# Kernel tuning notes

Measured on AMD Instinct MI355X. Metric: run time of the kernel, lower is better.

Reference implementation:

```python
import math
import jax, jax.numpy as jnp
import numpy as np

B, S, D, H, L, V = 2, 1024, 1024, 16, 6, 256
HD = D // H  # 64
PAD = 0


def setup_inputs() -> dict:
    key = jax.random.key(0)
    ks = jax.random.split(key, 22)
    s = 0.02
    f32 = jnp.float32
    inp = {
        "x": jax.random.randint(ks[0], (B, S), 0, V, dtype=jnp.int32),
        "emb": (jax.random.normal(ks[1], (V, D)) * s).astype(f32),
        "Wq": (jax.random.normal(ks[2], (L, D, D)) * s).astype(f32),
        "bq": jnp.zeros((L, D), f32),
        "Wk": (jax.random.normal(ks[3], (L, D, D)) * s).astype(f32),
        "bk": jnp.zeros((L, D), f32),
        "Wv": (jax.random.normal(ks[4], (L, D, D)) * s).astype(f32),
        "bv": jnp.zeros((L, D), f32),
        "Wo": (jax.random.normal(ks[5], (L, D, D)) * s).astype(f32),
        "bo": jnp.zeros((L, D), f32),
        "W1": (jax.random.normal(ks[6], (L, D, D // 2)) * s).astype(f32),
        "b1": jnp.zeros((L, D // 2), f32),
        "W2": (jax.random.normal(ks[7], (L, D // 2, D)) * s).astype(f32),
        "b2": jnp.zeros((L, D), f32),
        "g1": jnp.ones((L, D), f32),
        "be1": jnp.zeros((L, D), f32),
        "g2": jnp.ones((L, D), f32),
        "be2": jnp.zeros((L, D), f32),
        "E": jax.random.normal(ks[8], (L, S, HD)).astype(f32),  # relative pos embeddings, non-trainable
        "Wf": (jax.random.normal(ks[9], (D, V)) * s).astype(f32),
        "bf": jnp.zeros((V,), f32),
    }
    return inp


def _layernorm(x, g, b, eps=1e-6):
    mu = jnp.mean(x, axis=-1, keepdims=True)
    var = jnp.mean((x - mu) ** 2, axis=-1, keepdims=True)
    return (x - mu) * jax.lax.rsqrt(var + eps) * g + b


def _pos_encoding():
    # embed[p, i] = sin(p * exp(-ln(1e4)*i/D) * exp(ln(1e4)*(i%2)/D) + 0.5*pi*(i%2))
    i = jnp.arange(D, dtype=jnp.float32)
    par = jnp.mod(i, 2.0)
    rate = jnp.exp(-math.log(10000.0) * i / D) * jnp.exp(math.log(10000.0) * par / D)
    pos = jnp.arange(S, dtype=jnp.float32)
    return jnp.sin(pos[:, None] * rate[None, :] + 0.5 * math.pi * par[None, :])  # [S, D]


def _skew(QE):
    # Music Transformer skewing: pad one col on the left, reshape, drop first row.
    padded = jnp.pad(QE, ((0, 0), (0, 0), (0, 0), (1, 0)))  # [B,H,S,S+1]
    reshaped = padded.reshape(B, H, S + 1, S)
    return reshaped[:, :, 1:, :]  # [B,H,S,S]


def reference(x, emb, Wq, bq, Wk, bk, Wv, bv, Wo, bo, W1, b1, W2, b2,
              g1, be1, g2, be2, E, Wf, bf):
    pe = _pos_encoding()
    # look-ahead mask: pad positions OR strictly-future positions
    pad_mask = (x == PAD)[:, None, None, :]                      # [B,1,1,S]
    causal = jnp.triu(jnp.ones((S, S), bool), k=1)[None, None]   # [1,1,S,S]
    neg = (pad_mask | causal).astype(jnp.float32) * -1e9         # [B,1,S,S]
    # QE mask: keep qe[i, j] only where j >= S-1-i (upper-right triangle)
    idx = jnp.arange(S)
    qe_mask = (idx[None, :] >= (S - 1 - idx)[:, None]).astype(jnp.float32)

    h = emb[x] * math.sqrt(D) + pe[None]  # [B,S,D]
    scale = 1.0 / math.sqrt(HD)
    for l in range(L):
        q = (h @ Wq[l] + bq[l]).reshape(B, S, H, HD).transpose(0, 2, 1, 3)
        k = (h @ Wk[l] + bk[l]).reshape(B, S, H, HD).transpose(0, 2, 1, 3)
        v = (h @ Wv[l] + bv[l]).reshape(B, S, H, HD).transpose(0, 2, 1, 3)
        QE = jnp.einsum('bhld,md->bhlm', q, E[l]) * qe_mask
        Srel = _skew(QE)
        logits = (jnp.einsum('bhld,bhmd->bhlm', q, k) + Srel) * scale + neg
        aw = jax.nn.softmax(logits, axis=-1)
        attn = jnp.einsum('bhlm,bhmd->bhld', aw, v)
        attn = attn.transpose(0, 2, 1, 3).reshape(B, S, D)
        ao = attn @ Wo[l] + bo[l]
        o1 = _layernorm(ao, g1[l], be1[l])          # NOTE: no residual, as in source
        f = jax.nn.relu(o1 @ W1[l] + b1[l]) @ W2[l] + b2[l]
        h = _layernorm(f, g2[l], be2[l])
    return h @ Wf + bf  # [B,S,V]
```

## Files before the change

kernel.cpp:

```cpp
#include <hip/hip_runtime.h>
#include <hip/hip_bf16.h>


typedef __attribute__((ext_vector_type(8))) short  s8_t;
typedef __attribute__((ext_vector_type(4))) short  s4_t;
typedef __attribute__((ext_vector_type(8))) __bf16 bf8_t;
typedef __attribute__((ext_vector_type(4))) float  f4v;

static __device__ __forceinline__ short f2bf(float f) {
  union { float f; unsigned u; } a; a.f = f;
  unsigned u = a.u;
  u += 0x7fffu + ((u >> 16) & 1u);
  return (short)(u >> 16);
}
static __device__ __forceinline__ float bf2f(short s) {
  union { float f; unsigned u; } a;
  a.u = ((unsigned)(unsigned short)s) << 16;
  return a.f;
}
static __device__ __forceinline__ f4v mfma16(s8_t a, s8_t b, f4v c) {
  return __builtin_amdgcn_mfma_f32_16x16x32_bf16(
      __builtin_bit_cast(bf8_t, a), __builtin_bit_cast(bf8_t, b), c, 0, 0, 0);
}
static __device__ __forceinline__ void gld16(const short* g, short* l) {
  __builtin_amdgcn_global_load_lds(
      (const __attribute__((address_space(1))) void*)g,
      (__attribute__((address_space(3))) void*)l, 16, 0, 0);
}

static __device__ const int IT_TAB[40] = {
  15,15,15,15, 14,14,14,14, 13,13,13,13, 12,12,12,12,
  11,11,11, 10,10,10, 9,9,9, 8,8,8,
  7,7, 6,6, 5,5, 4,4, 3, 2, 1, 0};
static __device__ const int CW_TAB[40] = {
  0,1,2,3, 0,1,2,3, 0,1,2,3, 0,1,2,3,
  0,1,2, 0,1,2, 0,1,2, 0,1,2,
  0,1, 0,1, 0,1, 0,1, 0, 0, 0, 0};

__global__ void prep_weights(
    const float* __restrict__ Wq, const float* __restrict__ Wk,
    const float* __restrict__ Wv, const float* __restrict__ Wo,
    const float* __restrict__ W1, const float* __restrict__ W2,
    const float* __restrict__ Wf,
    short* __restrict__ qkvT, short* __restrict__ WoT, short* __restrict__ W1T,
    short* __restrict__ W2T, short* __restrict__ WfT) {
  __shared__ float tile[32][33];
  int z = blockIdx.x;
  const float* in; short* out; int R, C; long outBS; int rowOff = 0;
  if (z < 18432) {
    R = 1024; C = 1024; outBS = (long)3072 * 1024; out = qkvT;
    if (z < 6144)       { in = Wq; }
    else if (z < 12288) { in = Wk; rowOff = 1024; z -= 6144; }
    else                { in = Wv; rowOff = 2048; z -= 12288; }
  } else if (z < 24576) { in = Wo; out = WoT; R = 1024; C = 1024; outBS = (long)1024 * 1024; z -= 18432; }
  else if (z < 27648)   { in = W1; out = W1T; R = 1024; C = 512;  outBS = (long)512 * 1024;  z -= 24576; }
  else if (z < 30720)   { in = W2; out = W2T; R = 512;  C = 1024; outBS = (long)1024 * 512;  z -= 27648; }
  else                  { in = Wf; out = WfT; R = 1024; C = 256;  outBS = 0;                 z -= 30720; }
  const int nx = C >> 5, ny = R >> 5;
  const int per = nx * ny;
  const int l = z / per, rem = z % per;
  const int cx = rem % nx, cy = rem / nx;
  in += (long)l * R * C;
  out += (long)l * outBS + (long)rowOff * R;
  const int c0 = cx * 32, r0 = cy * 32;
  const int tx = threadIdx.x, ty = threadIdx.y;
#pragma unroll
  for (int i = 0; i < 4; i++)
    tile[ty + i * 8][tx] = in[(long)(r0 + ty + i * 8) * C + c0 + tx];
  __syncthreads();
#pragma unroll
  for (int i = 0; i < 4; i++)
    out[(long)(c0 + ty + i * 8) * R + r0 + tx] = f2bf(tile[tx][ty + i * 8]);
}

__global__ __launch_bounds__(256) void prep_misc(
    const int* __restrict__ x, const float* __restrict__ emb,
    const float* __restrict__ E,
    const float* __restrict__ bq, const float* __restrict__ bk,
    const float* __restrict__ bv,
    short* __restrict__ h, short* __restrict__ Ebf,
    float* __restrict__ qkvB, int* __restrict__ fnp) {
  const int z = blockIdx.x;
  const int tid = threadIdx.x;
  if (z < 2048) {
    const int s = z & 1023;
    const int xv = x[z];
    const int c = tid << 2;
    const float4 e = *(const float4*)(emb + (long)xv * 1024 + c);
    const float ev[4] = {e.x, e.y, e.z, e.w};
    s4_t o;
#pragma unroll
    for (int i = 0; i < 4; i++) {
      const int d = c + i;
      const float par = (float)(d & 1);
      const float rate = expf(-9.210340371976184f * (float)d / 1024.0f) *
                         expf(9.210340371976184f * par / 1024.0f);
      const float pe = sinf((float)s * rate + 1.5707963267948966f * par);
      o[i] = f2bf(ev[i] * 32.0f + pe);
    }
    *(s4_t*)(h + (long)z * 1024 + c) = o;
  } else if (z < 2432) {
    const long i = ((long)(z - 2048) * 256 + tid) * 4;
    const float4 t = *(const float4*)(E + i);
    s4_t o = {f2bf(t.x), f2bf(t.y), f2bf(t.z), f2bf(t.w)};
    *(s4_t*)(Ebf + i) = o;
  } else if (z < 2504) {
    const int idx = (z - 2432) * 256 + tid;
    const int l = idx / 3072, n = idx % 3072;
    float v = (n < 1024) ? bq[l * 1024 + n]
            : (n < 2048) ? bk[l * 1024 + n - 1024]
                         : bv[l * 1024 + n - 2048];
    qkvB[idx] = v;
  } else {
    if (tid < 64) {
      const int b = z - 2504;
      int first = 1024;
      for (int j0 = 0; j0 < 1024; j0 += 64) {
        unsigned long long m = __ballot(x[b * 1024 + j0 + tid] != 0);
        if (m) { first = j0 + __ffsll(m) - 1; break; }
      }
      if (tid == 0) fnp[b] = first;
    }
  }
}

__global__ __launch_bounds__(256) void ln_kernel(const short* __restrict__ in,
                                                 short* __restrict__ out,
                                                 const float* __restrict__ g,
                                                 const float* __restrict__ be) {
  __shared__ float red[4];
  __shared__ float red2[4];
  const int row = blockIdx.x;
  const int tid = threadIdx.x;
  const int c = tid << 2;
  const s4_t xv = *(const s4_t*)(in + (long)row * 1024 + c);
  const float x0 = bf2f(xv[0]), x1 = bf2f(xv[1]), x2 = bf2f(xv[2]), x3 = bf2f(xv[3]);
  float s = x0 + x1 + x2 + x3;
#pragma unroll
  for (int off = 1; off < 64; off <<= 1) s += __shfl_xor(s, off);
  const int wave = tid >> 6, lane = tid & 63;
  if (lane == 0) red[wave] = s;
  __syncthreads();
  const float mu = (red[0] + red[1] + red[2] + red[3]) * (1.0f / 1024.0f);
  const float d0 = x0 - mu, d1 = x1 - mu, d2 = x2 - mu, d3 = x3 - mu;
  float q = d0 * d0 + d1 * d1 + d2 * d2 + d3 * d3;
#pragma unroll
  for (int off = 1; off < 64; off <<= 1) q += __shfl_xor(q, off);
  if (lane == 0) red2[wave] = q;
  __syncthreads();
  const float var = (red2[0] + red2[1] + red2[2] + red2[3]) * (1.0f / 1024.0f);
  const float rs = rsqrtf(var + 1e-6f);
  const float4 gv = *(const float4*)(g + c);
  const float4 bv = *(const float4*)(be + c);
  s4_t o = {f2bf(d0 * rs * gv.x + bv.x), f2bf(d1 * rs * gv.y + bv.y),
            f2bf(d2 * rs * gv.z + bv.z), f2bf(d3 * rs * gv.w + bv.w)};
  *(s4_t*)(out + (long)row * 1024 + c) = o;
}

template <int BM, int BN, int WR, int WC, int OUT_BF16, int RELU>
__global__ __launch_bounds__(256) void gemm_lds(
    const short* __restrict__ A, const short* __restrict__ BT,
    void* __restrict__ Cv, const float* __restrict__ biasp,
    int K, int lda, int ldb, int ldc) {
  constexpr int AR = BM / 64, BR = BN / 64;
  constexpr int FI = BM / WR / 16, FJ = BN / WC / 16;
  __shared__ short As[BM * 32];
  __shared__ short Bs[BN * 32];
  const int bm = blockIdx.y * BM, bn = blockIdx.x * BN;
  const int tid = threadIdx.x;
  const int wave = tid >> 6, lane = tid & 63;
  const int quad = lane >> 4, l16 = lane & 15;
  const int wr = wave / WC, wc = wave % WC;
  const int wm = wr * (BM / WR), wn = wc * (BN / WC);

  const short* Ag = A + (long)(bm + wave * 16 + (lane >> 2)) * lda + ((lane & 3) << 3);
  const short* Bg = BT + (long)(bn + wave * 16 + (lane >> 2)) * ldb + ((lane & 3) << 3);

  f4v acc[FI][FJ];
#pragma unroll
  for (int i = 0; i < FI; i++)
#pragma unroll
    for (int j = 0; j < FJ; j++) {
      f4v zz = {0.f, 0.f, 0.f, 0.f};
      acc[i][j] = zz;
    }

  for (int k0 = 0; k0 < K; k0 += 32) {
#pragma unroll
    for (int r = 0; r < AR; r++)
      gld16(Ag + (long)r * 64 * lda + k0, As + r * 2048 + wave * 512);
#pragma unroll
    for (int r = 0; r < BR; r++)
      gld16(Bg + (long)r * 64 * ldb + k0, Bs + r * 2048 + wave * 512);
    __syncthreads();
    s8_t af[FI], bfr[FJ];
#pragma unroll
    for (int t = 0; t < FI; t++)
      af[t] = *(const s8_t*)&As[(wm + t * 16 + l16) * 32 + quad * 8];
#pragma unroll
    for (int t = 0; t < FJ; t++)
      bfr[t] = *(const s8_t*)&Bs[(wn + t * 16 + l16) * 32 + quad * 8];
#pragma unroll
    for (int ti = 0; ti < FI; ti++)
#pragma unroll
      for (int tj = 0; tj < FJ; tj++)
        acc[ti][tj] = mfma16(af[ti], bfr[tj], acc[ti][tj]);
    __syncthreads();
  }

#pragma unroll
  for (int ti = 0; ti < FI; ti++) {
#pragma unroll
    for (int tj = 0; tj < FJ; tj++) {
      const int n = bn + wn + tj * 16 + l16;
      const float bval = biasp ? biasp[n] : 0.f;
#pragma unroll
      for (int r = 0; r < 4; r++) {
        const int m = bm + wm + ti * 16 + quad * 4 + r;
        float vv = acc[ti][tj][r] + bval;
        if (RELU) vv = fmaxf(vv, 0.f);
        if (OUT_BF16) ((short*)Cv)[(long)m * ldc + n] = f2bf(vv);
        else          ((float*)Cv)[(long)m * ldc + n] = vv;
      }
    }
  }
}

__global__ __launch_bounds__(256) void attn_main(
    const short* __restrict__ qkv, const short* __restrict__ Eb,
    const int* __restrict__ xids, const int* __restrict__ fnp,
    float* __restrict__ PO, float* __restrict__ PM, float* __restrict__ PL,
    short* __restrict__ outb) {
  __shared__ short Ks2[8][64][8];
  __shared__ short Vt[64][72];
  __shared__ short Gs[4][16][88];
  __shared__ float kneg[64];

  const int bh = blockIdx.x, b = bh >> 4, hh = bh & 15;
  const int yy = blockIdx.y;
  const bool fbp = (yy >= 40);
  const int itile = fbp ? (yy - 40) : IT_TAB[yy];
  const int cw = fbp ? 0 : CW_TAB[yy];
  const int fb = fnp[b];
  const int i0g = itile * 64;
  if (fbp && fb <= i0g) return;

  const int tid = threadIdx.x;
  const int wave = tid >> 6, lane = tid & 63, quad = lane >> 4, l16 = lane & 15;
  const int i0 = i0g + wave * 16;

  s8_t aq[2];
  {
    const short* qp = qkv + ((long)(b * 1024 + i0 + l16)) * 3072 + hh * 64 + quad * 8;
    aq[0] = *(const s8_t*)qp;
    aq[1] = *(const s8_t*)(qp + 32);
  }

  f4v o[4];
#pragma unroll
  for (int nt = 0; nt < 4; nt++) { f4v zz = {0.f, 0.f, 0.f, 0.f}; o[nt] = zz; }
  float m_run[4] = {-INFINITY, -INFINITY, -INFINITY, -INFINITY};
  float l_run[4] = {0.f, 0.f, 0.f, 0.f};

  const short* kbase = qkv + (long)b * 1024 * 3072 + 1024 + hh * 64 + wave * 8;
  const short* vbase = qkv + (long)b * 1024 * 3072 + 2048 + hh * 64 + wave * 16;
  short* gs = &Gs[wave][0][0];

  const int jBeg = fbp ? 0 : cw * 256;
  const int jEnd = fbp ? 1024 : min(cw * 256 + 256, i0g + 64);

  for (int j0 = jBeg; j0 < jEnd; j0 += 64) {
    {
      const long k1 = min(j0 + lane, 1023);
      gld16(kbase + k1 * 3072, &Ks2[wave][0][0]);
      gld16(kbase + k1 * 3072 + 32, &Ks2[wave + 4][0][0]);
      const short* vrow = vbase + k1 * 3072;
      const s8_t v0 = *(const s8_t*)(vrow);
      const s8_t v1 = *(const s8_t*)(vrow + 8);
#pragma unroll
      for (int t = 0; t < 8; t++) {
        Vt[wave * 16 + t][lane] = v0[t];
        Vt[wave * 16 + 8 + t][lane] = v1[t];
      }
    }
    if (tid < 64) kneg[tid] = (xids[b * 1024 + min(j0 + tid, 1023)] == 0) ? -1e9f : 0.0f;

    {
      const int mW = 1008 - i0g - wave * 16 + j0;
#pragma unroll
      for (int t = 0; t < 5; t++) {
        const int m = min(mW + t * 16 + l16, 1023);
        const short* ep = Eb + m * 64 + quad * 8;
        const s8_t eb0 = *(const s8_t*)ep;
        const s8_t eb1 = *(const s8_t*)(ep + 32);
        f4v g = {0.f, 0.f, 0.f, 0.f};
        g = mfma16(aq[0], eb0, g);
        g = mfma16(aq[1], eb1, g);
#pragma unroll
        for (int r = 0; r < 4; r++)
          gs[(quad * 4 + r) * 88 + t * 16 + l16] = f2bf(g[r]);
      }
    }
    __syncthreads();

    float p[4][4];
    const int irow = i0 + quad * 4;
#pragma unroll
    for (int jt = 0; jt < 4; jt++) {
      const s8_t k0f = *(const s8_t*)&Ks2[quad][jt * 16 + l16][0];
      const s8_t k1f = *(const s8_t*)&Ks2[4 + quad][jt * 16 + l16][0];
      f4v zz = {0.f, 0.f, 0.f, 0.f};
      zz = mfma16(aq[0], k0f, zz);
      zz = mfma16(aq[1], k1f, zz);
      const int j = j0 + jt * 16 + l16;
      const float kn = kneg[jt * 16 + l16];
#pragma unroll
      for (int r = 0; r < 4; r++) {
        const int rr = quad * 4 + r;
        const float smv = bf2f(gs[rr * 87 + 15 + jt * 16 + l16]);
        const bool causal = (j <= irow + r);
        const float srel = causal ? smv : 0.f;
        const float kk = fbp ? 0.f : (causal ? kn : -1e9f);
        p[jt][r] = (zz[r] + srel) * 0.125f + kk;
      }
    }

    float alpha[4];
#pragma unroll
    for (int r = 0; r < 4; r++) {
      float mx = p[0][r];
#pragma unroll
      for (int jt = 1; jt < 4; jt++) mx = fmaxf(mx, p[jt][r]);
      mx = fmaxf(mx, __shfl_xor(mx, 1));
      mx = fmaxf(mx, __shfl_xor(mx, 2));
      mx = fmaxf(mx, __shfl_xor(mx, 4));
      mx = fmaxf(mx, __shfl_xor(mx, 8));
      const float mnew = fmaxf(m_run[r], mx);
      alpha[r] = __expf(m_run[r] - mnew);
      float ps = 0.f;
#pragma unroll
      for (int jt = 0; jt < 4; jt++) {
        p[jt][r] = __expf(p[jt][r] - mnew);
        ps += p[jt][r];
      }
      ps += __shfl_xor(ps, 1);
      ps += __shfl_xor(ps, 2);
      ps += __shfl_xor(ps, 4);
      ps += __shfl_xor(ps, 8);
      l_run[r] = l_run[r] * alpha[r] + ps;
      m_run[r] = mnew;
    }

#pragma unroll
    for (int jt = 0; jt < 4; jt++)
#pragma unroll
      for (int r = 0; r < 4; r++)
        gs[(quad * 4 + r) * 88 + jt * 16 + l16] = f2bf(p[jt][r]);
#pragma unroll
    for (int nt = 0; nt < 4; nt++)
#pragma unroll
      for (int r = 0; r < 4; r++)
        o[nt][r] *= alpha[r];

#pragma unroll
    for (int ks4 = 0; ks4 < 2; ks4++) {
      const s8_t ap = *(const s8_t*)&gs[l16 * 88 + ks4 * 32 + quad * 8];
#pragma unroll
      for (int nt = 0; nt < 4; nt++) {
        const s8_t vf = *(const s8_t*)&Vt[nt * 16 + l16][ks4 * 32 + quad * 8];
        o[nt] = mfma16(ap, vf, o[nt]);
      }
    }
    __syncthreads();
  }

  if (fbp) {
#pragma unroll
    for (int nt = 0; nt < 4; nt++)
#pragma unroll
      for (int r = 0; r < 4; r++) {
        const int i = i0 + quad * 4 + r;
        if (i < fb)
          outb[((long)(b * 1024 + i)) * 1024 + hh * 64 + nt * 16 + l16] =
              f2bf(o[nt][r] / l_run[r]);
      }
  } else if (yy >= 36) {
#pragma unroll
    for (int nt = 0; nt < 4; nt++)
#pragma unroll
      for (int r = 0; r < 4; r++) {
        const int i = i0 + quad * 4 + r;
        if (i >= fb)
          outb[((long)(b * 1024 + i)) * 1024 + hh * 64 + nt * 16 + l16] =
              f2bf(o[nt][r] / l_run[r]);
      }
  } else {
    const long part = (long)(bh * 16 + itile) * 4 + cw;
    float* po = PO + part * 4096;
#pragma unroll
    for (int nt = 0; nt < 4; nt++)
#pragma unroll
      for (int r = 0; r < 4; r++) {
        const int row = wave * 16 + quad * 4 + r;
        po[row * 64 + nt * 16 + l16] = o[nt][r];
      }
    if (l16 == 0) {
#pragma unroll
      for (int r = 0; r < 4; r++) {
        const int row = wave * 16 + quad * 4 + r;
        PM[part * 64 + row] = m_run[r];
        PL[part * 64 + row] = l_run[r];
      }
    }
  }
}

__global__ __launch_bounds__(256) void attn_combine(
    const float* __restrict__ PO, const float* __restrict__ PM,
    const float* __restrict__ PL, const int* __restrict__ fnp,
    short* __restrict__ outb) {
  const int id = blockIdx.x;
  const int bh = id / 12, itile = 4 + id % 12;
  const int b = bh >> 4, hh = bh & 15;
  const int nc = (itile >> 2) + 1;
  const int row = threadIdx.x >> 2, seg = (threadIdx.x & 3) << 4;
  const long base = (long)(bh * 16 + itile) * 4;
  const int i = itile * 64 + row;
  if (i < fnp[b]) return;

  float mv[4];
  float M = -INFINITY;
  for (int c = 0; c < nc; c++) {
    mv[c] = PM[(base + c) * 64 + row];
    M = fmaxf(M, mv[c]);
  }
  f4v acc[4];
#pragma unroll
  for (int t = 0; t < 4; t++) { f4v zz = {0.f, 0.f, 0.f, 0.f}; acc[t] = zz; }
  float l = 0.f;
  for (int c = 0; c < nc; c++) {
    const float w = __expf(mv[c] - M);
    l += w * PL[(base + c) * 64 + row];
    const float* po = PO + (base + c) * 4096 + row * 64 + seg;
#pragma unroll
    for (int t = 0; t < 4; t++) {
      const f4v v = *(const f4v*)(po + t * 4);
      acc[t] += w * v;
    }
  }
  const float inv = 1.0f / l;
  short* op = outb + ((long)(b * 1024 + i)) * 1024 + hh * 64 + seg;
#pragma unroll
  for (int t = 0; t < 4; t++) {
    s4_t o = {f2bf(acc[t][0] * inv), f2bf(acc[t][1] * inv),
              f2bf(acc[t][2] * inv), f2bf(acc[t][3] * inv)};
    *(s4_t*)(op + t * 4) = o;
  }
}

extern "C" void kernel_launch(void* const* d_in, const int* in_sizes, int n_in,
                              void* d_out, int out_size, void* d_ws, size_t ws_size,
                              hipStream_t stream) {
  const int*   x   = (const int*)d_in[0];
  const float* emb = (const float*)d_in[1];
  const float* Wq  = (const float*)d_in[2];
  const float* bq  = (const float*)d_in[3];
  const float* Wk  = (const float*)d_in[4];
  const float* bk  = (const float*)d_in[5];
  const float* Wv  = (const float*)d_in[6];
  const float* bv  = (const float*)d_in[7];
  const float* Wo  = (const float*)d_in[8];
  const float* bo  = (const float*)d_in[9];
  const float* W1  = (const float*)d_in[10];
  const float* b1  = (const float*)d_in[11];
  const float* W2  = (const float*)d_in[12];
  const float* b2  = (const float*)d_in[13];
  const float* g1  = (const float*)d_in[14];
  const float* be1 = (const float*)d_in[15];
  const float* g2  = (const float*)d_in[16];
  const float* be2 = (const float*)d_in[17];
  const float* E   = (const float*)d_in[18];
  const float* Wf  = (const float*)d_in[19];
  const float* bfv = (const float*)d_in[20];

  char* p = (char*)d_ws;
  auto alloc = [&](size_t bytes) {
    char* r = p;
    p += (bytes + 255) & ~(size_t)255;
    return r;
  };
  short* h    = (short*)alloc(2048ull * 1024 * 2);
  short* qkv  = (short*)alloc(2048ull * 3072 * 2);
  short* attn = (short*)alloc(2048ull * 1024 * 2);
  short* tmp  = (short*)alloc(2048ull * 1024 * 2);
  short* mid  = (short*)alloc(2048ull * 512 * 2);
  short* qkvT = (short*)alloc(6ull * 3072 * 1024 * 2);
  short* WoT  = (short*)alloc(6ull * 1024 * 1024 * 2);
  short* W1T  = (short*)alloc(6ull * 512 * 1024 * 2);
  short* W2T  = (short*)alloc(6ull * 1024 * 512 * 2);
  short* WfT  = (short*)alloc(256ull * 1024 * 2);
  short* Ebf  = (short*)alloc(6ull * 1024 * 64 * 2);
  float* qkvB = (float*)alloc(6ull * 3072 * 4);
  int*   fnp  = (int*)alloc(256);
  float* PO   = (float*)alloc(2048ull * 4096 * 4);
  float* PM   = (float*)alloc(2048ull * 64 * 4);
  float* PL   = (float*)alloc(2048ull * 64 * 4);

  prep_weights<<<30976, dim3(32, 8), 0, stream>>>(
      Wq, Wk, Wv, Wo, W1, W2, Wf, qkvT, WoT, W1T, W2T, WfT);
  prep_misc<<<2506, 256, 0, stream>>>(x, emb, E, bq, bk, bv, h, Ebf, qkvB, fnp);

  for (int l = 0; l < 6; l++) {
    const long wOff = (long)l * 1024 * 1024;
    const long w12Off = (long)l * 512 * 1024;
    gemm_lds<128, 128, 2, 2, 1, 0><<<dim3(24, 16), 256, 0, stream>>>(
        h, qkvT + (long)l * 3072 * 1024, qkv, qkvB + l * 3072, 1024, 1024, 1024, 3072);
    attn_main<<<dim3(32, 56), 256, 0, stream>>>(
        qkv, Ebf + (long)l * 1024 * 64, x, fnp, PO, PM, PL, attn);
    attn_combine<<<384, 256, 0, stream>>>(PO, PM, PL, fnp, attn);
    gemm_lds<64, 64, 2, 2, 1, 0><<<dim3(16, 32), 256, 0, stream>>>(
        attn, WoT + wOff, tmp, bo + l * 1024, 1024, 1024, 1024, 1024);
    ln_kernel<<<2048, 256, 0, stream>>>(tmp, tmp, g1 + l * 1024, be1 + l * 1024);
    gemm_lds<64, 64, 2, 2, 1, 1><<<dim3(8, 32), 256, 0, stream>>>(
        tmp, W1T + w12Off, mid, b1 + l * 512, 1024, 1024, 1024, 512);
    gemm_lds<64, 64, 2, 2, 1, 0><<<dim3(16, 32), 256, 0, stream>>>(
        mid, W2T + w12Off, h, b2 + l * 1024, 512, 512, 512, 1024);
    ln_kernel<<<2048, 256, 0, stream>>>(h, h, g2 + l * 1024, be2 + l * 1024);
  }
  gemm_lds<64, 64, 2, 2, 0, 0><<<dim3(4, 32), 256, 0, stream>>>(
      h, WfT, (float*)d_out, bfv, 1024, 1024, 1024, 256);
}
```

Baseline: 968.4 us.

## Double-buffer K/V tiles in attention and widen weight-transpose tiles

The attention kernel now double-buffers the K tile in shared memory and prefetches the next V rows into registers while the current tile is computed, so global loads overlap with MFMA work. The key-padding mask is precomputed once per block as a bf16 array covering the whole sequence instead of being reloaded every iteration. The weight-prep transpose moves to 64x64 tiles with float4 loads and 16-byte bf16 stores, cutting the block count. This costs more LDS and registers per block, which could lower occupancy, and the bf16 mask value of -1e9 is no longer exact.

```diff
diff --git a/kernel.cpp b/kernel.cpp
--- a/kernel.cpp
+++ b/kernel.cpp
@@ -37,40 +37,54 @@
   0,1,2, 0,1,2, 0,1,2, 0,1,2,
   0,1, 0,1, 0,1, 0,1, 0, 0, 0, 0};
 
-__global__ void prep_weights(
+__global__ __launch_bounds__(256) void prep_weights(
     const float* __restrict__ Wq, const float* __restrict__ Wk,
     const float* __restrict__ Wv, const float* __restrict__ Wo,
     const float* __restrict__ W1, const float* __restrict__ W2,
     const float* __restrict__ Wf,
     short* __restrict__ qkvT, short* __restrict__ WoT, short* __restrict__ W1T,
     short* __restrict__ W2T, short* __restrict__ WfT) {
-  __shared__ float tile[32][33];
+  __shared__ float tile[64][69];
   int z = blockIdx.x;
   const float* in; short* out; int R, C; long outBS; int rowOff = 0;
-  if (z < 18432) {
+  if (z < 4608) {
     R = 1024; C = 1024; outBS = (long)3072 * 1024; out = qkvT;
-    if (z < 6144)       { in = Wq; }
-    else if (z < 12288) { in = Wk; rowOff = 1024; z -= 6144; }
-    else                { in = Wv; rowOff = 2048; z -= 12288; }
-  } else if (z < 24576) { in = Wo; out = WoT; R = 1024; C = 1024; outBS = (long)1024 * 1024; z -= 18432; }
-  else if (z < 27648)   { in = W1; out = W1T; R = 1024; C = 512;  outBS = (long)512 * 1024;  z -= 24576; }
-  else if (z < 30720)   { in = W2; out = W2T; R = 512;  C = 1024; outBS = (long)1024 * 512;  z -= 27648; }
-  else                  { in = Wf; out = WfT; R = 1024; C = 256;  outBS = 0;                 z -= 30720; }
-  const int nx = C >> 5, ny = R >> 5;
+    if (z < 1536)      { in = Wq; }
+    else if (z < 3072) { in = Wk; rowOff = 1024; z -= 1536; }
+    else               { in = Wv; rowOff = 2048; z -= 3072; }
+  } else if (z < 6144) { in = Wo; out = WoT; R = 1024; C = 1024; outBS = (long)1024 * 1024; z -= 4608; }
+  else if (z < 6912)   { in = W1; out = W1T; R = 1024; C = 512;  outBS = (long)512 * 1024;  z -= 6144; }
+  else if (z < 7680)   { in = W2; out = W2T; R = 512;  C = 1024; outBS = (long)1024 * 512;  z -= 6912; }
+  else                 { in = Wf; out = WfT; R = 1024; C = 256;  outBS = 0;                 z -= 7680; }
+  const int nx = C >> 6, ny = R >> 6;
   const int per = nx * ny;
   const int l = z / per, rem = z % per;
   const int cx = rem % nx, cy = rem / nx;
   in += (long)l * R * C;
   out += (long)l * outBS + (long)rowOff * R;
-  const int c0 = cx * 32, r0 = cy * 32;
-  const int tx = threadIdx.x, ty = threadIdx.y;
-#pragma unroll
-  for (int i = 0; i < 4; i++)
-    tile[ty + i * 8][tx] = in[(long)(r0 + ty + i * 8) * C + c0 + tx];
+  const int c0 = cx * 64, r0 = cy * 64;
+  const int tid = threadIdx.x;
+
+  const int lr = tid >> 4, lc4 = tid & 15;
+#pragma unroll
+  for (int p = 0; p < 4; p++) {
+    const int row = p * 16 + lr;
+    const float4 v = *(const float4*)(in + (long)(r0 + row) * C + c0 + lc4 * 4);
+    tile[row][lc4 * 4 + 0] = v.x;
+    tile[row][lc4 * 4 + 1] = v.y;
+    tile[row][lc4 * 4 + 2] = v.z;
+    tile[row][lc4 * 4 + 3] = v.w;
+  }
   __syncthreads();
-#pragma unroll
-  for (int i = 0; i < 4; i++)
-    out[(long)(c0 + ty + i * 8) * R + r0 + tx] = f2bf(tile[tx][ty + i * 8]);
+  const int seg = tid & 7;
+#pragma unroll
+  for (int q = 0; q < 2; q++) {
+    const int oc = q * 32 + (tid >> 3);
+    s8_t o;
+#pragma unroll
+    for (int j = 0; j < 8; j++) o[j] = f2bf(tile[seg * 8 + j][oc]);
+    *(s8_t*)(out + (long)(c0 + oc) * R + r0 + seg * 8) = o;
+  }
 }
 
 __global__ __launch_bounds__(256) void prep_misc(
@@ -231,10 +245,10 @@
     const int* __restrict__ xids, const int* __restrict__ fnp,
     float* __restrict__ PO, float* __restrict__ PM, float* __restrict__ PL,
     short* __restrict__ outb) {
-  __shared__ short Ks2[8][64][8];
+  __shared__ short Ks2[2][8][64][8];
   __shared__ short Vt[64][72];
   __shared__ short Gs[4][16][88];
-  __shared__ float kneg[64];
+  __shared__ short knegs[1024];
 
   const int bh = blockIdx.x, b = bh >> 4, hh = bh & 15;
   const int yy = blockIdx.y;
@@ -249,6 +263,15 @@
   const int wave = tid >> 6, lane = tid & 63, quad = lane >> 4, l16 = lane & 15;
   const int i0 = i0g + wave * 16;
 
+  {
+    const short neg = f2bf(-1e9f);
+#pragma unroll
+    for (int t = 0; t < 4; t++) {
+      const int idx = t * 256 + tid;
+      knegs[idx] = (xids[b * 1024 + idx] == 0) ? neg : (short)0;
+    }
+  }
+
   s8_t aq[2];
   {
     const short* qp = qkv + ((long)(b * 1024 + i0 + l16)) * 3072 + hh * 64 + quad * 8;
@@ -269,21 +292,25 @@
   const int jBeg = fbp ? 0 : cw * 256;
   const int jEnd = fbp ? 1024 : min(cw * 256 + 256, i0g + 64);
 
+  s8_t vr0, vr1;
+  {
+    const long k1 = min(jBeg + lane, 1023);
+    gld16(kbase + k1 * 3072, &Ks2[0][wave][0][0]);
+    gld16(kbase + k1 * 3072 + 32, &Ks2[0][wave + 4][0][0]);
+    const short* vrow = vbase + k1 * 3072;
+    vr0 = *(const s8_t*)(vrow);
+    vr1 = *(const s8_t*)(vrow + 8);
+#pragma unroll
+    for (int t = 0; t < 8; t++) {
+      Vt[wave * 16 + t][lane] = vr0[t];
+      Vt[wave * 16 + 8 + t][lane] = vr1[t];
+    }
+  }
+
+  int pb = 0;
   for (int j0 = jBeg; j0 < jEnd; j0 += 64) {
-    {
-      const long k1 = min(j0 + lane, 1023);
-      gld16(kbase + k1 * 3072, &Ks2[wave][0][0]);
-      gld16(kbase + k1 * 3072 + 32, &Ks2[wave + 4][0][0]);
-      const short* vrow = vbase + k1 * 3072;
-      const s8_t v0 = *(const s8_t*)(vrow);
-      const s8_t v1 = *(const s8_t*)(vrow + 8);
-#pragma unroll
-      for (int t = 0; t < 8; t++) {
-        Vt[wave * 16 + t][lane] = v0[t];
-        Vt[wave * 16 + 8 + t][lane] = v1[t];
-      }
-    }
-    if (tid < 64) kneg[tid] = (xids[b * 1024 + min(j0 + tid, 1023)] == 0) ? -1e9f : 0.0f;
+    const bool hasNext = (j0 + 64 < jEnd);
+    __syncthreads();
 
     {
       const int mW = 1008 - i0g - wave * 16 + j0;
@@ -301,19 +328,27 @@
           gs[(quad * 4 + r) * 88 + t * 16 + l16] = f2bf(g[r]);
       }
     }
-    __syncthreads();
+
+    if (hasNext) {
+      const long k1 = min(j0 + 64 + lane, 1023);
+      gld16(kbase + k1 * 3072, &Ks2[pb ^ 1][wave][0][0]);
+      gld16(kbase + k1 * 3072 + 32, &Ks2[pb ^ 1][wave + 4][0][0]);
+      const short* vrow = vbase + k1 * 3072;
+      vr0 = *(const s8_t*)(vrow);
+      vr1 = *(const s8_t*)(vrow + 8);
+    }
 
     float p[4][4];
     const int irow = i0 + quad * 4;
 #pragma unroll
     for (int jt = 0; jt < 4; jt++) {
-      const s8_t k0f = *(const s8_t*)&Ks2[quad][jt * 16 + l16][0];
-      const s8_t k1f = *(const s8_t*)&Ks2[4 + quad][jt * 16 + l16][0];
+      const s8_t k0f = *(const s8_t*)&Ks2[pb][quad][jt * 16 + l16][0];
+      const s8_t k1f = *(const s8_t*)&Ks2[pb][4 + quad][jt * 16 + l16][0];
       f4v zz = {0.f, 0.f, 0.f, 0.f};
       zz = mfma16(aq[0], k0f, zz);
       zz = mfma16(aq[1], k1f, zz);
       const int j = j0 + jt * 16 + l16;
-      const float kn = kneg[jt * 16 + l16];
+      const float kn = bf2f(knegs[j]);
 #pragma unroll
       for (int r = 0; r < 4; r++) {
         const int rr = quad * 4 + r;
@@ -371,7 +406,16 @@
         o[nt] = mfma16(ap, vf, o[nt]);
       }
     }
+
     __syncthreads();
+    if (hasNext) {
+#pragma unroll
+      for (int t = 0; t < 8; t++) {
+        Vt[wave * 16 + t][lane] = vr0[t];
+        Vt[wave * 16 + 8 + t][lane] = vr1[t];
+      }
+    }
+    pb ^= 1;
   }
 
   if (fbp) {
@@ -506,7 +550,7 @@
   float* PM   = (float*)alloc(2048ull * 64 * 4);
   float* PL   = (float*)alloc(2048ull * 64 * 4);
 
-  prep_weights<<<30976, dim3(32, 8), 0, stream>>>(
+  prep_weights<<<7744, 256, 0, stream>>>(
       Wq, Wk, Wv, Wo, W1, W2, Wf, qkvT, WoT, W1T, W2T, WfT);
   prep_misc<<<2506, 256, 0, stream>>>(x, emb, E, bq, bk, bv, h, Ebf, qkvB, fnp);
 
```

Measured after the change: 973.5 us. Within noise of the previous version (+0.5%).
